# Performance work log

Hardware: AMD Instinct MI355X
Metric: run time of the kernel (lower is better)

## Reference

```python
import jax, jax.numpy as jnp
import numpy as np

B, H, S, D = 8, 12, 1024, 64

def setup_inputs() -> dict:
    key = jax.random.key(0)
    kq, kk, kv = jax.random.split(key, 3)
    q = jax.random.normal(kq, (B, H, S, D), dtype=jnp.float32)
    k = jax.random.normal(kk, (B, H, S, D), dtype=jnp.float32)
    v = jax.random.normal(kv, (B, H, S, D), dtype=jnp.float32)
    scale = 8  # sqrt(d_head)
    return {"q": q, "k": k, "v": v, "scale": scale}

def reference(q, k, v, scale):
    # scores: (B,H,S,S) = q @ k^T / scale, softmax over last axis
    scores = jnp.einsum('bhqd,bhkd->bhqk', q, k) / scale
    attention_score = jax.nn.softmax(scores, axis=-1)
    # context: (B,H,S,D)
    attention_context = jnp.einsum('bhqk,bhkd->bhqd', attention_score, v)
    return (attention_score, attention_context)
```

## Files before the change

### kernel.cpp

```cpp
#include <hip/hip_runtime.h>


#define SLEN 1024
#define DHEAD 64
#define NBH 96
#define QROWS 16

typedef __attribute__((ext_vector_type(4))) float f32x4;
typedef __attribute__((ext_vector_type(4))) __bf16 bf16x4;
typedef __attribute__((ext_vector_type(8))) __bf16 bf16x8;

union BF8 { bf16x8 v; bf16x4 h[2]; };

#define KB_ELEMS ((size_t)NBH * SLEN * DHEAD)
#define WS_BYTES (KB_ELEMS * 2 * 2)

__device__ __forceinline__ int keyof(int tau) {
  return 32 * (tau >> 5) + ((tau >> 3) & 3) * 4 + 16 * ((tau >> 2) & 1) + (tau & 3);
}

__global__ __launch_bounds__(256)
void prepass(const float* __restrict__ Kp, const float* __restrict__ Vp,
             __bf16* __restrict__ Kb, __bf16* __restrict__ VTb) {
  __shared__ float tf[64][68];
  const int b = blockIdx.x, t = threadIdx.x;
  if (b < 1536) {
    const int bh = b >> 4, kc = b & 15;
    const float* Vg = Vp + ((size_t)bh * SLEN + (size_t)kc * 64) * DHEAD;
    #pragma unroll
    for (int i = 0; i < 4; ++i) {
      int r = i * 16 + (t >> 4), d0 = (t & 15) * 4;
      f32x4 v = *(const f32x4*)(Vg + (size_t)r * DHEAD + d0);
      #pragma unroll
      for (int j = 0; j < 4; ++j) tf[r][d0 + j] = v[j];
    }
    __syncthreads();
    const int d = t >> 2, tb = (t & 3) * 16;
    __bf16* dst = VTb + ((size_t)bh * DHEAD + d) * SLEN + kc * 64 + tb;
    BF8 o0, o1;
    #pragma unroll
    for (int x = 0; x < 8; ++x) {
      o0.v[x] = (__bf16)tf[keyof(tb + x)][d];
      o1.v[x] = (__bf16)tf[keyof(tb + 8 + x)][d];
    }
    *(bf16x8*)dst = o0.v;
    *(bf16x8*)(dst + 8) = o1.v;
  } else {
    const size_t base = (size_t)(b - 1536) * 4096;
    #pragma unroll
    for (int i = 0; i < 4; ++i) {
      size_t off = base + i * 1024 + t * 4;
      f32x4 v = *(const f32x4*)(Kp + off);
      bf16x4 o;
      #pragma unroll
      for (int j = 0; j < 4; ++j) o[j] = (__bf16)v[j];
      *(bf16x4*)(Kb + off) = o;
    }
  }
}

struct SMem {
  __bf16 qt[QROWS][80];
  float red_m[4][16];
  float red_s[4][16];
  union {
    float ctxr[4][QROWS][72];
    float plin[2][QROWS][268];
  } u;
};

template<bool STAGED>
__global__ __launch_bounds__(256, 4)
void attn_main(const float* __restrict__ Qp, const float* __restrict__ Kp,
               const float* __restrict__ Vp, const __bf16* __restrict__ Kb,
               const __bf16* __restrict__ VTb, const int* __restrict__ scale_p,
               float* __restrict__ out) {
  __shared__ SMem sm;
  const int tid  = threadIdx.x;
  const int w    = tid >> 6;
  const int lane = tid & 63;
  const int quad = lane >> 4;
  const int c16  = lane & 15;

  const int bid   = blockIdx.x;
  const int slot  = bid >> 3;
  const int bh    = (bid & 7) * 12 + (slot >> 6);
  const int qbase = (slot & 63) * QROWS;

  int siv = *scale_p;
  float fs = (siv >= 1 && siv <= (1 << 24)) ? (float)siv : __int_as_float(siv);
  const float inv_scale = 1.0f / fs;

  {
    int r = tid >> 4, d0 = (tid & 15) * 4;
    f32x4 qv = *(const f32x4*)(Qp + ((size_t)bh * SLEN + qbase + r) * DHEAD + d0);
    bf16x4 o;
    #pragma unroll
    for (int j = 0; j < 4; ++j) o[j] = (__bf16)(qv[j] * inv_scale);
    *(bf16x4*)&sm.qt[r][d0] = o;
  }
  __syncthreads();

  BF8 qf0, qf1;
  qf0.v = *(const bf16x8*)&sm.qt[c16][quad * 8];
  qf1.v = *(const bf16x8*)&sm.qt[c16][32 + quad * 8];

  f32x4 acc[16];
  {
    f32x4 z = {0.0f, 0.0f, 0.0f, 0.0f};
    #pragma unroll
    for (int mt = 0; mt < 16; ++mt) acc[mt] = z;
  }
  const __bf16* Kbbase = STAGED ? Kb + ((size_t)bh * SLEN + w * 256) * DHEAD : nullptr;
  const float*  Kfbase = Kp + ((size_t)bh * SLEN + (size_t)w * 256) * DHEAD;
  #pragma unroll
  for (int mt = 0; mt < 16; ++mt) {
    int row = mt * 16 + c16;
    bf16x8 a0, a1;
    if constexpr (STAGED) {
      a0 = *(const bf16x8*)(Kbbase + (size_t)row * DHEAD + quad * 8);
      a1 = *(const bf16x8*)(Kbbase + (size_t)row * DHEAD + 32 + quad * 8);
    } else {
      const float* kr = Kfbase + (size_t)row * DHEAD + quad * 8;
      f32x4 x0 = *(const f32x4*)(kr);
      f32x4 x1 = *(const f32x4*)(kr + 4);
      f32x4 y0 = *(const f32x4*)(kr + 32);
      f32x4 y1 = *(const f32x4*)(kr + 36);
      #pragma unroll
      for (int j = 0; j < 4; ++j) {
        a0[j] = (__bf16)x0[j]; a0[j + 4] = (__bf16)x1[j];
        a1[j] = (__bf16)y0[j]; a1[j + 4] = (__bf16)y1[j];
      }
    }
    acc[mt] = __builtin_amdgcn_mfma_f32_16x16x32_bf16(a0, qf0.v, acc[mt], 0, 0, 0);
    acc[mt] = __builtin_amdgcn_mfma_f32_16x16x32_bf16(a1, qf1.v, acc[mt], 0, 0, 0);
  }

  float m;
  {
    float a = fmaxf(fmaxf(acc[0][0], acc[0][1]), fmaxf(acc[0][2], acc[0][3]));
    #pragma unroll
    for (int mt = 1; mt < 16; ++mt) {
      float b2 = fmaxf(fmaxf(acc[mt][0], acc[mt][1]), fmaxf(acc[mt][2], acc[mt][3]));
      a = fmaxf(a, b2);
    }
    a = fmaxf(a, __shfl_xor(a, 16));
    a = fmaxf(a, __shfl_xor(a, 32));
    if (lane < 16) sm.red_m[w][c16] = a;
  }
  __syncthreads();
  m = fmaxf(fmaxf(sm.red_m[0][c16], sm.red_m[1][c16]),
            fmaxf(sm.red_m[2][c16], sm.red_m[3][c16]));

  float s = 0.0f;
  #pragma unroll
  for (int mt = 0; mt < 16; ++mt)
    #pragma unroll
    for (int j = 0; j < 4; ++j) {
      float e = __expf(acc[mt][j] - m);
      acc[mt][j] = e;
      s += e;
    }
  s += __shfl_xor(s, 16);
  s += __shfl_xor(s, 32);
  if (lane < 16) sm.red_s[w][c16] = s;
  __syncthreads();
  const float inv = 1.0f / (sm.red_s[0][c16] + sm.red_s[1][c16] +
                            sm.red_s[2][c16] + sm.red_s[3][c16]);

  BF8 pf[8];
  #pragma unroll
  for (int mt = 0; mt < 16; ++mt) {
    #pragma unroll
    for (int j = 0; j < 4; ++j) {
      float p = acc[mt][j] * inv;
      acc[mt][j] = p;
      pf[mt >> 1].v[(mt & 1) * 4 + j] = (__bf16)p;
    }
  }

  f32x4 ctx[4];
  {
    f32x4 z = {0.0f, 0.0f, 0.0f, 0.0f};
    #pragma unroll
    for (int dt = 0; dt < 4; ++dt) ctx[dt] = z;
  }
  const __bf16* Vt = STAGED ? VTb + (size_t)bh * DHEAD * SLEN : nullptr;
  #pragma unroll
  for (int t8 = 0; t8 < 8; ++t8) {
    #pragma unroll
    for (int dt = 0; dt < 4; ++dt) {
      BF8 b;
      if constexpr (STAGED) {
        b.v = *(const bf16x8*)(Vt + (size_t)(dt * 16 + c16) * SLEN +
                               w * 256 + t8 * 32 + quad * 8);
      } else {
        int k0 = w * 256 + t8 * 32 + quad * 4;
        #pragma unroll
        for (int j = 0; j < 8; ++j)
          b.v[j] = (__bf16)Vp[((size_t)bh * SLEN + k0 + (j & 3) + 16 * (j >> 2)) * DHEAD +
                              dt * 16 + c16];
      }
      ctx[dt] = __builtin_amdgcn_mfma_f32_16x16x32_bf16(pf[t8].v, b.v, ctx[dt], 0, 0, 0);
    }
  }

  #pragma unroll
  for (int dt = 0; dt < 4; ++dt)
    #pragma unroll
    for (int i = 0; i < 4; ++i)
      sm.u.ctxr[w][quad * 4 + i][dt * 16 + c16] = ctx[dt][i];
  __syncthreads();
  {
    int q = tid >> 4, d4 = (tid & 15) * 4;
    f32x4 r0 = *(const f32x4*)&sm.u.ctxr[0][q][d4];
    f32x4 r1 = *(const f32x4*)&sm.u.ctxr[1][q][d4];
    f32x4 r2 = *(const f32x4*)&sm.u.ctxr[2][q][d4];
    f32x4 r3 = *(const f32x4*)&sm.u.ctxr[3][q][d4];
    f32x4 o;
    #pragma unroll
    for (int j = 0; j < 4; ++j) o[j] = (r0[j] + r1[j]) + (r2[j] + r3[j]);
    float* outC = out + (size_t)NBH * SLEN * SLEN;
    *(f32x4*)(outC + ((size_t)bh * SLEN + qbase + q) * DHEAD + d4) = o;
  }
  __syncthreads();

  #pragma unroll
  for (int r = 0; r < 2; ++r) {
    if ((w >> 1) == r) {
      #pragma unroll
      for (int mt = 0; mt < 16; ++mt)
        *(f32x4*)&sm.u.plin[w & 1][c16][mt * 16 + quad * 4] = acc[mt];
    }
    __syncthreads();
    #pragma unroll
    for (int jj = 0; jj < 8; ++jj) {
      int idx = w * 8 + jj;
      int h = idx >> 4, row = idx & 15;
      f32x4 vls = *(const f32x4*)&sm.u.plin[h][row][lane * 4];
      *(f32x4*)(out + ((size_t)bh * SLEN + qbase + row) * SLEN +
                (size_t)(r * 2 + h) * 256 + lane * 4) = vls;
    }
    if (r == 0) __syncthreads();
  }
}

extern "C" void kernel_launch(void* const* d_in, const int* in_sizes, int n_in,
                              void* d_out, int out_size, void* d_ws, size_t ws_size,
                              hipStream_t stream) {
  (void)in_sizes; (void)n_in; (void)out_size;
  const float* q = (const float*)d_in[0];
  const float* k = (const float*)d_in[1];
  const float* v = (const float*)d_in[2];
  const int* scale = (const int*)d_in[3];
  float* out = (float*)d_out;

  const bool staged = (d_ws != nullptr) && (ws_size >= (size_t)WS_BYTES);
  dim3 block(256);
  if (staged) {
    __bf16* Kb  = (__bf16*)d_ws;
    __bf16* VTb = Kb + KB_ELEMS;
    hipLaunchKernelGGL(prepass, dim3(3072), block, 0, stream, k, v, Kb, VTb);
    hipLaunchKernelGGL(attn_main<true>, dim3((SLEN / QROWS) * NBH), block, 0, stream,
                       q, k, v, Kb, VTb, scale, out);
  } else {
    hipLaunchKernelGGL(attn_main<false>, dim3((SLEN / QROWS) * NBH), block, 0, stream,
                       q, k, v, (const __bf16*)nullptr, (const __bf16*)nullptr, scale, out);
  }
}
```

Before: 634.5 us.

## Use 8 waves per block and interleave score stores with PV MFMAs

Doubles the block to 512 threads so each wave handles 128 keys instead of 256, halving per-thread accumulator registers. The normalized probability tile is written to a full-width shared buffer once, and its global stores are interleaved with the P·V MFMA loop rather than done in a separate serialized two-pass phase afterward. It also adds s_setprio around MFMA groups. Shared memory per block grows to about 66KB for the 16x1028 buffer, which may limit blocks per CU, and the context reduction now sums 8 partials.

```diff
diff --git a/kernel.cpp b/kernel.cpp
--- a/kernel.cpp
+++ b/kernel.cpp
@@ -60,17 +60,17 @@
 }
 
 struct SMem {
+  union {
+    float plin[QROWS][1028];
+    float ctxr[8][QROWS][68];
+  } u;
   __bf16 qt[QROWS][80];
-  float red_m[4][16];
-  float red_s[4][16];
-  union {
-    float ctxr[4][QROWS][72];
-    float plin[2][QROWS][268];
-  } u;
+  float red_m[8][16];
+  float red_s[8][16];
 };
 
 template<bool STAGED>
-__global__ __launch_bounds__(256, 4)
+__global__ __launch_bounds__(512, 4)
 void attn_main(const float* __restrict__ Qp, const float* __restrict__ Kp,
                const float* __restrict__ Vp, const __bf16* __restrict__ Kb,
                const __bf16* __restrict__ VTb, const int* __restrict__ scale_p,
@@ -91,7 +91,7 @@
   float fs = (siv >= 1 && siv <= (1 << 24)) ? (float)siv : __int_as_float(siv);
   const float inv_scale = 1.0f / fs;
 
-  {
+  if (tid < 256) {
     int r = tid >> 4, d0 = (tid & 15) * 4;
     f32x4 qv = *(const f32x4*)(Qp + ((size_t)bh * SLEN + qbase + r) * DHEAD + d0);
     bf16x4 o;
@@ -105,16 +105,16 @@
   qf0.v = *(const bf16x8*)&sm.qt[c16][quad * 8];
   qf1.v = *(const bf16x8*)&sm.qt[c16][32 + quad * 8];
 
-  f32x4 acc[16];
+  f32x4 acc[8];
   {
     f32x4 z = {0.0f, 0.0f, 0.0f, 0.0f};
     #pragma unroll
-    for (int mt = 0; mt < 16; ++mt) acc[mt] = z;
-  }
-  const __bf16* Kbbase = STAGED ? Kb + ((size_t)bh * SLEN + w * 256) * DHEAD : nullptr;
-  const float*  Kfbase = Kp + ((size_t)bh * SLEN + (size_t)w * 256) * DHEAD;
-  #pragma unroll
-  for (int mt = 0; mt < 16; ++mt) {
+    for (int mt = 0; mt < 8; ++mt) acc[mt] = z;
+  }
+  const __bf16* Kbbase = STAGED ? Kb + ((size_t)bh * SLEN + w * 128) * DHEAD : nullptr;
+  const float*  Kfbase = Kp + ((size_t)bh * SLEN + (size_t)w * 128) * DHEAD;
+  #pragma unroll
+  for (int mt = 0; mt < 8; ++mt) {
     int row = mt * 16 + c16;
     bf16x8 a0, a1;
     if constexpr (STAGED) {
@@ -132,15 +132,17 @@
         a1[j] = (__bf16)y0[j]; a1[j + 4] = (__bf16)y1[j];
       }
     }
+    __builtin_amdgcn_s_setprio(1);
     acc[mt] = __builtin_amdgcn_mfma_f32_16x16x32_bf16(a0, qf0.v, acc[mt], 0, 0, 0);
     acc[mt] = __builtin_amdgcn_mfma_f32_16x16x32_bf16(a1, qf1.v, acc[mt], 0, 0, 0);
+    __builtin_amdgcn_s_setprio(0);
   }
 
   float m;
   {
     float a = fmaxf(fmaxf(acc[0][0], acc[0][1]), fmaxf(acc[0][2], acc[0][3]));
     #pragma unroll
-    for (int mt = 1; mt < 16; ++mt) {
+    for (int mt = 1; mt < 8; ++mt) {
       float b2 = fmaxf(fmaxf(acc[mt][0], acc[mt][1]), fmaxf(acc[mt][2], acc[mt][3]));
       a = fmaxf(a, b2);
     }
@@ -149,12 +151,17 @@
     if (lane < 16) sm.red_m[w][c16] = a;
   }
   __syncthreads();
-  m = fmaxf(fmaxf(sm.red_m[0][c16], sm.red_m[1][c16]),
-            fmaxf(sm.red_m[2][c16], sm.red_m[3][c16]));
+  {
+    float m0 = fmaxf(sm.red_m[0][c16], sm.red_m[1][c16]);
+    float m1 = fmaxf(sm.red_m[2][c16], sm.red_m[3][c16]);
+    float m2 = fmaxf(sm.red_m[4][c16], sm.red_m[5][c16]);
+    float m3 = fmaxf(sm.red_m[6][c16], sm.red_m[7][c16]);
+    m = fmaxf(fmaxf(m0, m1), fmaxf(m2, m3));
+  }
 
   float s = 0.0f;
   #pragma unroll
-  for (int mt = 0; mt < 16; ++mt)
+  for (int mt = 0; mt < 8; ++mt)
     #pragma unroll
     for (int j = 0; j < 4; ++j) {
       float e = __expf(acc[mt][j] - m);
@@ -165,19 +172,23 @@
   s += __shfl_xor(s, 32);
   if (lane < 16) sm.red_s[w][c16] = s;
   __syncthreads();
-  const float inv = 1.0f / (sm.red_s[0][c16] + sm.red_s[1][c16] +
-                            sm.red_s[2][c16] + sm.red_s[3][c16]);
-
-  BF8 pf[8];
-  #pragma unroll
-  for (int mt = 0; mt < 16; ++mt) {
-    #pragma unroll
-    for (int j = 0; j < 4; ++j) {
-      float p = acc[mt][j] * inv;
-      acc[mt][j] = p;
-      pf[mt >> 1].v[(mt & 1) * 4 + j] = (__bf16)p;
-    }
-  }
+  const float inv = 1.0f / (((sm.red_s[0][c16] + sm.red_s[1][c16]) +
+                             (sm.red_s[2][c16] + sm.red_s[3][c16])) +
+                            ((sm.red_s[4][c16] + sm.red_s[5][c16]) +
+                             (sm.red_s[6][c16] + sm.red_s[7][c16])));
+
+  BF8 pf[4];
+  #pragma unroll
+  for (int mt = 0; mt < 8; ++mt) {
+    f32x4 p;
+    #pragma unroll
+    for (int j = 0; j < 4; ++j) p[j] = acc[mt][j] * inv;
+    *(f32x4*)&sm.u.plin[c16][w * 128 + mt * 16 + quad * 4] = p;
+    #pragma unroll
+    for (int j = 0; j < 4; ++j)
+      pf[mt >> 1].v[(mt & 1) * 4 + j] = (__bf16)p[j];
+  }
+  __syncthreads();
 
   f32x4 ctx[4];
   {
@@ -186,24 +197,38 @@
     for (int dt = 0; dt < 4; ++dt) ctx[dt] = z;
   }
   const __bf16* Vt = STAGED ? VTb + (size_t)bh * DHEAD * SLEN : nullptr;
-  #pragma unroll
-  for (int t8 = 0; t8 < 8; ++t8) {
-    #pragma unroll
-    for (int dt = 0; dt < 4; ++dt) {
-      BF8 b;
-      if constexpr (STAGED) {
-        b.v = *(const bf16x8*)(Vt + (size_t)(dt * 16 + c16) * SLEN +
-                               w * 256 + t8 * 32 + quad * 8);
-      } else {
-        int k0 = w * 256 + t8 * 32 + quad * 4;
+  const int srow2 = tid >> 8;
+  const int scol4 = (tid & 255) * 4;
+  #pragma unroll
+  for (int t8 = 0; t8 < 4; ++t8) {
+    BF8 b[4];
+    if constexpr (STAGED) {
+      #pragma unroll
+      for (int dt = 0; dt < 4; ++dt)
+        b[dt].v = *(const bf16x8*)(Vt + (size_t)(dt * 16 + c16) * SLEN +
+                                   w * 128 + t8 * 32 + quad * 8);
+    } else {
+      int k0 = w * 128 + t8 * 32 + quad * 4;
+      #pragma unroll
+      for (int dt = 0; dt < 4; ++dt)
         #pragma unroll
         for (int j = 0; j < 8; ++j)
-          b.v[j] = (__bf16)Vp[((size_t)bh * SLEN + k0 + (j & 3) + 16 * (j >> 2)) * DHEAD +
-                              dt * 16 + c16];
-      }
-      ctx[dt] = __builtin_amdgcn_mfma_f32_16x16x32_bf16(pf[t8].v, b.v, ctx[dt], 0, 0, 0);
-    }
-  }
+          b[dt].v[j] = (__bf16)Vp[((size_t)bh * SLEN + k0 + (j & 3) + 16 * (j >> 2)) * DHEAD +
+                                  dt * 16 + c16];
+    }
+    #pragma unroll
+    for (int h = 0; h < 2; ++h) {
+      int row = (t8 * 2 + h) * 2 + srow2;
+      f32x4 vls = *(const f32x4*)&sm.u.plin[row][scol4];
+      *(f32x4*)(out + ((size_t)bh * SLEN + qbase + row) * SLEN + scol4) = vls;
+    }
+    __builtin_amdgcn_s_setprio(1);
+    #pragma unroll
+    for (int dt = 0; dt < 4; ++dt)
+      ctx[dt] = __builtin_amdgcn_mfma_f32_16x16x32_bf16(pf[t8].v, b[dt].v, ctx[dt], 0, 0, 0);
+    __builtin_amdgcn_s_setprio(0);
+  }
+  __syncthreads();
 
   #pragma unroll
   for (int dt = 0; dt < 4; ++dt)
@@ -211,37 +236,17 @@
     for (int i = 0; i < 4; ++i)
       sm.u.ctxr[w][quad * 4 + i][dt * 16 + c16] = ctx[dt][i];
   __syncthreads();
-  {
+  if (tid < 256) {
     int q = tid >> 4, d4 = (tid & 15) * 4;
-    f32x4 r0 = *(const f32x4*)&sm.u.ctxr[0][q][d4];
-    f32x4 r1 = *(const f32x4*)&sm.u.ctxr[1][q][d4];
-    f32x4 r2 = *(const f32x4*)&sm.u.ctxr[2][q][d4];
-    f32x4 r3 = *(const f32x4*)&sm.u.ctxr[3][q][d4];
-    f32x4 o;
-    #pragma unroll
-    for (int j = 0; j < 4; ++j) o[j] = (r0[j] + r1[j]) + (r2[j] + r3[j]);
+    f32x4 o = *(const f32x4*)&sm.u.ctxr[0][q][d4];
+    #pragma unroll
+    for (int w2 = 1; w2 < 8; ++w2) {
+      f32x4 r = *(const f32x4*)&sm.u.ctxr[w2][q][d4];
+      #pragma unroll
+      for (int j = 0; j < 4; ++j) o[j] += r[j];
+    }
     float* outC = out + (size_t)NBH * SLEN * SLEN;
     *(f32x4*)(outC + ((size_t)bh * SLEN + qbase + q) * DHEAD + d4) = o;
-  }
-  __syncthreads();
-
-  #pragma unroll
-  for (int r = 0; r < 2; ++r) {
-    if ((w >> 1) == r) {
-      #pragma unroll
-      for (int mt = 0; mt < 16; ++mt)
-        *(f32x4*)&sm.u.plin[w & 1][c16][mt * 16 + quad * 4] = acc[mt];
-    }
-    __syncthreads();
-    #pragma unroll
-    for (int jj = 0; jj < 8; ++jj) {
-      int idx = w * 8 + jj;
-      int h = idx >> 4, row = idx & 15;
-      f32x4 vls = *(const f32x4*)&sm.u.plin[h][row][lane * 4];
-      *(f32x4*)(out + ((size_t)bh * SLEN + qbase + row) * SLEN +
-                (size_t)(r * 2 + h) * 256 + lane * 4) = vls;
-    }
-    if (r == 0) __syncthreads();
   }
 }
 
@@ -256,15 +261,14 @@
   float* out = (float*)d_out;
 
   const bool staged = (d_ws != nullptr) && (ws_size >= (size_t)WS_BYTES);
-  dim3 block(256);
   if (staged) {
     __bf16* Kb  = (__bf16*)d_ws;
     __bf16* VTb = Kb + KB_ELEMS;
-    hipLaunchKernelGGL(prepass, dim3(3072), block, 0, stream, k, v, Kb, VTb);
-    hipLaunchKernelGGL(attn_main<true>, dim3((SLEN / QROWS) * NBH), block, 0, stream,
+    hipLaunchKernelGGL(prepass, dim3(3072), dim3(256), 0, stream, k, v, Kb, VTb);
+    hipLaunchKernelGGL(attn_main<true>, dim3((SLEN / QROWS) * NBH), dim3(512), 0, stream,
                        q, k, v, Kb, VTb, scale, out);
   } else {
-    hipLaunchKernelGGL(attn_main<false>, dim3((SLEN / QROWS) * NBH), block, 0, stream,
+    hipLaunchKernelGGL(attn_main<false>, dim3((SLEN / QROWS) * NBH), dim3(512), 0, stream,
                        q, k, v, (const __bf16*)nullptr, (const __bf16*)nullptr, scale, out);
   }
 }
```

New measurement: 626.7 us. No clear change (-1.2%).
